# Kernel tuning notes

Hardware: AMD Instinct MI355X
Metric: run time of the kernel (lower is better)

## Reference

```python
import jax, jax.numpy as jnp
import numpy as np

N, E, IN_DIM, EMBED_DIM, HID_DIM = 10000, 320000, 128, 128, 64
NEG_SLOPE = 0.2


def setup_inputs() -> dict:
    key = jax.random.key(0)
    ks = jax.random.split(key, 7)
    x = jax.random.normal(ks[0], (N, IN_DIM), dtype=jnp.float32)
    edge_index = jax.random.randint(ks[1], (2, E), 0, N, dtype=jnp.int64)
    dense_w = jax.random.normal(ks[2], (IN_DIM, EMBED_DIM), dtype=jnp.float32) / np.sqrt(IN_DIM)
    dense_b = jnp.zeros((EMBED_DIM,), dtype=jnp.float32)
    gat_w = jax.random.normal(ks[3], (EMBED_DIM, HID_DIM), dtype=jnp.float32) / np.sqrt(EMBED_DIM)
    att_src = jax.random.normal(ks[4], (HID_DIM,), dtype=jnp.float32) * 0.1
    att_dst = jax.random.normal(ks[5], (HID_DIM,), dtype=jnp.float32) * 0.1
    gat_b = jnp.zeros((HID_DIM,), dtype=jnp.float32)
    return {"x": x, "edge_index": edge_index, "dense_w": dense_w, "dense_b": dense_b,
            "gat_w": gat_w, "att_src": att_src, "att_dst": att_dst, "gat_b": gat_b}


def reference(x, edge_index, dense_w, dense_b, gat_w, att_src, att_dst, gat_b):
    n = x.shape[0]
    # dense + relu
    h = jax.nn.relu(x @ dense_w + dense_b)            # [N, embed]
    # GATConv (heads=1): linear transform
    z = h @ gat_w                                     # [N, hid]
    # add self loops (PyG default)
    loops = jnp.arange(n, dtype=edge_index.dtype)
    src = jnp.concatenate([edge_index[0], loops])     # [E+N] message source j
    dst = jnp.concatenate([edge_index[1], loops])     # [E+N] message target i
    a_src = z @ att_src                               # [N]
    a_dst = z @ att_dst                               # [N]
    e = jax.nn.leaky_relu(a_src[src] + a_dst[dst], NEG_SLOPE)  # [E+N]
    # segment softmax over incoming edges of each target node
    m = jax.ops.segment_max(e, dst, num_segments=n)
    ex = jnp.exp(e - m[dst])
    denom = jax.ops.segment_sum(ex, dst, num_segments=n)
    alpha = ex / denom[dst]                           # [E+N]
    embed_x = jax.ops.segment_sum(alpha[:, None] * z[src], dst, num_segments=n) + gat_b  # [N, hid]
    # pairwise sigmoid similarity
    sim = jax.nn.sigmoid(embed_x @ embed_x.T)         # [N, N]
    return sim, embed_x
```

## Files before the change

### kernel.cpp

```cpp
#include <hip/hip_runtime.h>
#include <math.h>

#define N_NODES 10000
#define E_EDGES 320000
#define IN_DIM 128
#define EMB 128
#define HID 64
#define NEG_SLOPE 0.2f

typedef __attribute__((ext_vector_type(8))) short short8;
typedef __attribute__((ext_vector_type(4))) short short4_t;
typedef __attribute__((ext_vector_type(4))) float floatx4;
typedef __attribute__((ext_vector_type(4))) int   intx4;
typedef __attribute__((ext_vector_type(2))) int   intx2;

__device__ __forceinline__ short f2bf(float f) {
    unsigned u = __float_as_uint(f);
    unsigned r = u + 0x7fffu + ((u >> 16) & 1u);
    return (short)(r >> 16);
}

__device__ __forceinline__ float sigmoidf_fast(float v) {
    return __builtin_amdgcn_rcpf(1.f + __expf(-v));
}

__global__ __launch_bounds__(256) void dense_gat_kernel(
    const float* __restrict__ x, const float* __restrict__ dw,
    const float* __restrict__ db, const float* __restrict__ gw,
    const float* __restrict__ asv, const float* __restrict__ adv,
    float* __restrict__ z, float* __restrict__ a_src, float* __restrict__ a_dst)
{
    __shared__ float xs[16][IN_DIM];
    __shared__ float hs[16][EMB];
    __shared__ float wsm[32 * 128];
    const int t = threadIdx.x;
    const int row0 = blockIdx.x * 16;

    #pragma unroll
    for (int r = 0; r < 2; ++r) {
        const int idx = t + r * 256;
        const int row = idx >> 5, c4 = idx & 31;
        *(floatx4*)&xs[row][c4 * 4] =
            *(const floatx4*)&x[(row0 + row) * IN_DIM + c4 * 4];
    }

    const int col = t & 127, rb = (t >> 7) * 8;
    float acc[8];
    {
        const float bias = db[col];
        #pragma unroll
        for (int r = 0; r < 8; ++r) acc[r] = bias;
    }
    for (int ch = 0; ch < 4; ++ch) {
        __syncthreads();
        #pragma unroll
        for (int r = 0; r < 4; ++r) {
            const int idx = t + r * 256;
            const int row = idx >> 5, c4 = idx & 31;
            *(floatx4*)&wsm[row * 128 + c4 * 4] =
                *(const floatx4*)&dw[(ch * 32 + row) * EMB + c4 * 4];
        }
        __syncthreads();
        #pragma unroll
        for (int jg = 0; jg < 8; ++jg) {
            const int jb = jg * 4;
            floatx4 xr[8];
            #pragma unroll
            for (int r = 0; r < 8; ++r)
                xr[r] = *(const floatx4*)&xs[rb + r][ch * 32 + jb];
            float wv[4];
            #pragma unroll
            for (int k = 0; k < 4; ++k) wv[k] = wsm[(jb + k) * 128 + col];
            #pragma unroll
            for (int k = 0; k < 4; ++k)
                #pragma unroll
                for (int r = 0; r < 8; ++r) acc[r] = fmaf(xr[r][k], wv[k], acc[r]);
        }
    }
    #pragma unroll
    for (int r = 0; r < 8; ++r) hs[rb + r][col] = fmaxf(acc[r], 0.f);

    const int col2 = t & 63, rb2 = (t >> 6) * 4;
    float acc2[4] = {0.f, 0.f, 0.f, 0.f};
    for (int ch = 0; ch < 2; ++ch) {
        __syncthreads();
        #pragma unroll
        for (int r = 0; r < 4; ++r) {
            const int idx = t + r * 256;
            const int row = idx >> 4, c4 = idx & 15;
            *(floatx4*)&wsm[row * 64 + c4 * 4] =
                *(const floatx4*)&gw[(ch * 64 + row) * HID + c4 * 4];
        }
        __syncthreads();
        #pragma unroll
        for (int kg = 0; kg < 16; ++kg) {
            const int kb = kg * 4;
            floatx4 hr[4];
            #pragma unroll
            for (int r = 0; r < 4; ++r)
                hr[r] = *(const floatx4*)&hs[rb2 + r][ch * 64 + kb];
            float gv[4];
            #pragma unroll
            for (int k = 0; k < 4; ++k) gv[k] = wsm[(kb + k) * 64 + col2];
            #pragma unroll
            for (int k = 0; k < 4; ++k)
                #pragma unroll
                for (int r = 0; r < 4; ++r) acc2[r] = fmaf(hr[r][k], gv[k], acc2[r]);
        }
    }

    const float as_c = asv[col2], ad_c = adv[col2];
    #pragma unroll
    for (int r = 0; r < 4; ++r) {
        z[(row0 + rb2 + r) * HID + col2] = acc2[r];
        float ps = acc2[r] * as_c;
        float pd = acc2[r] * ad_c;
        #pragma unroll
        for (int off = 32; off > 0; off >>= 1) {
            ps += __shfl_down(ps, off, 64);
            pd += __shfl_down(pd, off, 64);
        }
        if ((t & 63) == 0) {
            a_src[row0 + rb2 + r] = ps;
            a_dst[row0 + rb2 + r] = pd;
        }
    }
}

__global__ __launch_bounds__(256) void count_kernel(
    const int* __restrict__ ei, int* __restrict__ cnt)
{
    const int e = blockIdx.x * blockDim.x + threadIdx.x;
    const int total = E_EDGES + N_NODES;
    if (e >= total) return;
    int s, d;
    if (e < E_EDGES) { s = ei[e]; d = ei[E_EDGES + e]; }
    else             { s = d = e - E_EDGES; }
    if ((unsigned)s >= N_NODES || (unsigned)d >= N_NODES) return;
    atomicAdd(&cnt[d], 1);
}

__global__ __launch_bounds__(256) void scan_kernel(
    const int* __restrict__ cnt, int* __restrict__ offs, int* __restrict__ cursor)
{
    __shared__ int scnt[10240];
    __shared__ int part[256];
    const int t = threadIdx.x;
    #pragma unroll
    for (int r = 0; r < 10; ++r) {
        const int i4 = t + r * 256;
        intx4 v = {0, 0, 0, 0};
        if (i4 < 2500) v = *(const intx4*)&cnt[i4 * 4];
        *(intx4*)&scnt[i4 * 4] = v;
    }
    __syncthreads();
    const int base = t * 40;
    int vals[40];
    int local = 0;
    #pragma unroll
    for (int i = 0; i < 40; ++i) { vals[i] = scnt[base + i]; local += vals[i]; }
    part[t] = local;
    __syncthreads();
    for (int off = 1; off < 256; off <<= 1) {
        const int v = (t >= off) ? part[t - off] : 0;
        __syncthreads();
        part[t] += v;
        __syncthreads();
    }
    int running = (t == 0) ? 0 : part[t - 1];
    #pragma unroll
    for (int i = 0; i < 40; ++i) {
        const int idx = base + i;
        if (idx < N_NODES) { offs[idx] = running; cursor[idx] = running; }
        running += vals[i];
    }
    if (t == 255) offs[N_NODES] = running;
}

__global__ __launch_bounds__(256) void scatter_kernel(
    const int* __restrict__ ei, const float* __restrict__ a_src,
    const float* __restrict__ a_dst, int* __restrict__ cursor,
    intx2* __restrict__ se)
{
    const int e = blockIdx.x * blockDim.x + threadIdx.x;
    const int total = E_EDGES + N_NODES;
    if (e >= total) return;
    int s, d;
    if (e < E_EDGES) { s = ei[e]; d = ei[E_EDGES + e]; }
    else             { s = d = e - E_EDGES; }
    if ((unsigned)s >= N_NODES || (unsigned)d >= N_NODES) return;
    float v = a_src[s] + a_dst[d];
    v = (v > 0.f) ? v : NEG_SLOPE * v;
    const float w = __expf(v);
    const int pos = atomicAdd(&cursor[d], 1);
    intx2 p;
    p[0] = s;
    p[1] = __float_as_int(w);
    se[pos] = p;
}

__global__ __launch_bounds__(256) void aggregate_kernel(
    const int* __restrict__ offs, const intx2* __restrict__ se,
    const float* __restrict__ z, const float* __restrict__ gb,
    float* __restrict__ emb)
{
    const int wid  = (blockIdx.x * blockDim.x + threadIdx.x) >> 6;
    const int lane = threadIdx.x & 63;
    if (wid >= N_NODES) return;
    const int g  = lane >> 4;
    const int c4 = (lane & 15) * 4;
    const int beg = offs[wid], end = offs[wid + 1];
    floatx4 acc = {0.f, 0.f, 0.f, 0.f};
    float sw = 0.f;
    for (int i = beg + g; i < end; i += 4) {
        const intx2 p = se[i];
        const floatx4 zv = *(const floatx4*)&z[p[0] * HID + c4];
        const float w = __int_as_float(p[1]);
        acc += zv * w;
        sw  += w;
    }
    #pragma unroll
    for (int off = 16; off <= 32; off <<= 1) {
        #pragma unroll
        for (int k = 0; k < 4; ++k) acc[k] += __shfl_xor(acc[k], off, 64);
        sw += __shfl_xor(sw, off, 64);
    }
    if (g == 0) {
        const floatx4 gv = *(const floatx4*)&gb[c4];
        floatx4 r;
        #pragma unroll
        for (int k = 0; k < 4; ++k) r[k] = acc[k] / sw + gv[k];
        *(floatx4*)&emb[wid * HID + c4] = r;
    }
}

#define SROW 72
#define SCR_STRIDE 133
__global__ __launch_bounds__(256) void sim_kernel(
    const float* __restrict__ emb, float* __restrict__ sim)
{
    __shared__ float smem[128 * SCR_STRIDE];
    short* const As = (short*)smem;
    short* const Bs = (short*)smem + 128 * SROW;
    const int t    = threadIdx.x;
    const int lane = t & 63;
    const int wave = t >> 6;
    const int wm   = (wave >> 1) * 64;
    const int wn   = (wave & 1) * 64;
    const int l15  = lane & 15;
    const int quad = lane >> 4;

    int bi, bj;
    {
        const int gx = blockIdx.x, gy = blockIdx.y;
        if (gy <= gx) { bi = gy; bj = gx; }
        else          { bi = 40 + gx; bj = 79 + gx - gy; }
    }

    #pragma unroll
    for (int round = 0; round < 8; ++round) {
        const int idx = t + round * 256;
        const int row = idx >> 4, c4 = idx & 15;
        int gr = bi * 128 + row; if (gr > N_NODES - 1) gr = N_NODES - 1;
        int gc = bj * 128 + row; if (gc > N_NODES - 1) gc = N_NODES - 1;
        const floatx4 a = *(const floatx4*)&emb[gr * HID + c4 * 4];
        const floatx4 b = *(const floatx4*)&emb[gc * HID + c4 * 4];
        short4_t sa, sb;
        #pragma unroll
        for (int j = 0; j < 4; ++j) { sa[j] = f2bf(a[j]); sb[j] = f2bf(b[j]); }
        *(short4_t*)&As[row * SROW + c4 * 4] = sa;
        *(short4_t*)&Bs[row * SROW + c4 * 4] = sb;
    }
    __syncthreads();

    short8 afrag[4][2];
    #pragma unroll
    for (int ti = 0; ti < 4; ++ti)
        #pragma unroll
        for (int ks = 0; ks < 2; ++ks)
            afrag[ti][ks] = *(const short8*)&As[(wm + ti * 16 + l15) * SROW +
                                                ks * 32 + quad * 8];

    floatx4 acc[4][4];
    const floatx4 zero = {0.f, 0.f, 0.f, 0.f};
    #pragma unroll
    for (int ti = 0; ti < 4; ++ti)
        #pragma unroll
        for (int tj = 0; tj < 4; ++tj) acc[ti][tj] = zero;

    #pragma unroll
    for (int tj = 0; tj < 4; ++tj) {
        const short8 bf0 = *(const short8*)&Bs[(wn + tj * 16 + l15) * SROW + quad * 8];
        const short8 bf1 = *(const short8*)&Bs[(wn + tj * 16 + l15) * SROW + 32 + quad * 8];
        #pragma unroll
        for (int ti = 0; ti < 4; ++ti) {
            acc[ti][tj] = __builtin_amdgcn_mfma_f32_16x16x32_bf16(
                afrag[ti][0], bf0, acc[ti][tj], 0, 0, 0);
            acc[ti][tj] = __builtin_amdgcn_mfma_f32_16x16x32_bf16(
                afrag[ti][1], bf1, acc[ti][tj], 0, 0, 0);
        }
    }
    __syncthreads();

    #pragma unroll
    for (int ti = 0; ti < 4; ++ti)
        #pragma unroll
        for (int reg = 0; reg < 4; ++reg)
            #pragma unroll
            for (int tj = 0; tj < 4; ++tj)
                smem[(wm + ti * 16 + quad * 4 + reg) * SCR_STRIDE +
                     wn + tj * 16 + l15] = sigmoidf_fast(acc[ti][tj][reg]);
    __syncthreads();

    #pragma unroll
    for (int round = 0; round < 16; ++round) {
        const int idx = t + round * 256;
        const int rr = idx >> 5, cq = idx & 31;
        const int grow = bi * 128 + rr;
        const int gcol = bj * 128 + cq * 4;
        if (grow < N_NODES && gcol < N_NODES) {
            const floatx4 v4 = *(const floatx4*)&smem[rr * SCR_STRIDE + cq * 4];
            *(floatx4*)&sim[(unsigned)grow * N_NODES + gcol] = v4;
        }
    }
    if (bi != bj) {
        #pragma unroll
        for (int round = 0; round < 16; ++round) {
            const int idx = t + round * 256;
            const int rr = idx >> 5, cq = idx & 31;
            const int trow = bj * 128 + rr;
            const int tcol = bi * 128 + cq * 4;
            if (trow < N_NODES && tcol < N_NODES) {
                floatx4 v4;
                #pragma unroll
                for (int m = 0; m < 4; ++m)
                    v4[m] = smem[(cq * 4 + m) * SCR_STRIDE + rr];
                *(floatx4*)&sim[(unsigned)trow * N_NODES + tcol] = v4;
            }
        }
    }
}

extern "C" void kernel_launch(void* const* d_in, const int* in_sizes, int n_in,
                              void* d_out, int out_size, void* d_ws, size_t ws_size,
                              hipStream_t stream)
{
    const float* x   = (const float*)d_in[0];
    const int*   ei  = (const int*)d_in[1];
    const float* dw  = (const float*)d_in[2];
    const float* db  = (const float*)d_in[3];
    const float* gw  = (const float*)d_in[4];
    const float* asv = (const float*)d_in[5];
    const float* adv = (const float*)d_in[6];
    const float* gb  = (const float*)d_in[7];

    float* out = (float*)d_out;
    float* sim = out;
    float* emb = out + (size_t)N_NODES * N_NODES;

    const size_t need = 1350002u * sizeof(float);
    float* ws = (ws_size >= need) ? (float*)d_ws : out;
    float* z      = ws;
    float* a_src  = ws + 640000;
    float* a_dst  = ws + 650000;
    int*   cnt    = (int*)(ws + 660000);
    int*   offs   = (int*)(ws + 670000);
    int*   cursor = (int*)(ws + 680001);
    intx2* se     = (intx2*)(ws + 690002);

    hipMemsetAsync(cnt, 0, N_NODES * sizeof(int), stream);

    dense_gat_kernel<<<N_NODES / 16, 256, 0, stream>>>(x, dw, db, gw, asv, adv,
                                                       z, a_src, a_dst);

    const int total_edges = E_EDGES + N_NODES;
    const int eb = (total_edges + 255) / 256;
    count_kernel<<<eb, 256, 0, stream>>>(ei, cnt);
    scan_kernel<<<1, 256, 0, stream>>>(cnt, offs, cursor);
    scatter_kernel<<<eb, 256, 0, stream>>>(ei, a_src, a_dst, cursor, se);
    aggregate_kernel<<<(N_NODES * 64 + 255) / 256, 256, 0, stream>>>(
        offs, se, z, gb, emb);

    dim3 grid(79, 40);
    sim_kernel<<<grid, 256, 0, stream>>>(emb, sim);
}
```

Before: 563.9 us.

## Fuse graph stages into one cooperative kernel and use nontemporal sim stores

Merges the dense/GAT projection, edge counting, scan, scatter and aggregation into a single cooperative kernel with grid-wide syncs. Dense work and edge counting run concurrently on disjoint blocks. This removes several launch gaps and lets the two independent stages overlap, with a fallback to the old multi-kernel path if the cooperative launch fails. The sim output writes also become nontemporal stores to reduce cache pollution from the large N×N result. Risks include the cost of grid sync, lower occupancy from the launch bounds, and the single-block scan idling the rest of the grid.

```diff
diff --git a/kernel.cpp b/kernel.cpp
--- a/kernel.cpp
+++ b/kernel.cpp
@@ -1,5 +1,8 @@
 #include <hip/hip_runtime.h>
+#include <hip/hip_cooperative_groups.h>
 #include <math.h>
+
+namespace cg = cooperative_groups;
 
 #define N_NODES 10000
 #define E_EDGES 320000
@@ -8,6 +11,9 @@
 #define HID 64
 #define NEG_SLOPE 0.2f
 
+#define COOP_BLOCKS 1024
+#define DG_BLOCKS 625
+
 typedef __attribute__((ext_vector_type(8))) short short8;
 typedef __attribute__((ext_vector_type(4))) short short4_t;
 typedef __attribute__((ext_vector_type(4))) float floatx4;
@@ -24,23 +30,23 @@
     return __builtin_amdgcn_rcpf(1.f + __expf(-v));
 }
 
-__global__ __launch_bounds__(256) void dense_gat_kernel(
+__device__ __forceinline__ void dense_gat_body(
+    float* __restrict__ smem,
+    int row0, int t,
     const float* __restrict__ x, const float* __restrict__ dw,
     const float* __restrict__ db, const float* __restrict__ gw,
     const float* __restrict__ asv, const float* __restrict__ adv,
     float* __restrict__ z, float* __restrict__ a_src, float* __restrict__ a_dst)
 {
-    __shared__ float xs[16][IN_DIM];
-    __shared__ float hs[16][EMB];
-    __shared__ float wsm[32 * 128];
-    const int t = threadIdx.x;
-    const int row0 = blockIdx.x * 16;
+    float* const xs  = smem;
+    float* const hs  = smem + 2048;
+    float* const wsm = smem + 4096;
 
     #pragma unroll
     for (int r = 0; r < 2; ++r) {
         const int idx = t + r * 256;
         const int row = idx >> 5, c4 = idx & 31;
-        *(floatx4*)&xs[row][c4 * 4] =
+        *(floatx4*)&xs[row * 128 + c4 * 4] =
             *(const floatx4*)&x[(row0 + row) * IN_DIM + c4 * 4];
     }
 
@@ -67,7 +73,7 @@
             floatx4 xr[8];
             #pragma unroll
             for (int r = 0; r < 8; ++r)
-                xr[r] = *(const floatx4*)&xs[rb + r][ch * 32 + jb];
+                xr[r] = *(const floatx4*)&xs[(rb + r) * 128 + ch * 32 + jb];
             float wv[4];
             #pragma unroll
             for (int k = 0; k < 4; ++k) wv[k] = wsm[(jb + k) * 128 + col];
@@ -78,7 +84,7 @@
         }
     }
     #pragma unroll
-    for (int r = 0; r < 8; ++r) hs[rb + r][col] = fmaxf(acc[r], 0.f);
+    for (int r = 0; r < 8; ++r) hs[(rb + r) * 128 + col] = fmaxf(acc[r], 0.f);
 
     const int col2 = t & 63, rb2 = (t >> 6) * 4;
     float acc2[4] = {0.f, 0.f, 0.f, 0.f};
@@ -98,7 +104,7 @@
             floatx4 hr[4];
             #pragma unroll
             for (int r = 0; r < 4; ++r)
-                hr[r] = *(const floatx4*)&hs[rb2 + r][ch * 64 + kb];
+                hr[r] = *(const floatx4*)&hs[(rb2 + r) * 128 + ch * 64 + kb];
             float gv[4];
             #pragma unroll
             for (int k = 0; k < 4; ++k) gv[k] = wsm[(kb + k) * 64 + col2];
@@ -127,38 +133,33 @@
     }
 }
 
-__global__ __launch_bounds__(256) void count_kernel(
-    const int* __restrict__ ei, int* __restrict__ cnt)
-{
-    const int e = blockIdx.x * blockDim.x + threadIdx.x;
+__device__ __forceinline__ void count_body(
+    int tid, int nth, const int* __restrict__ ei, int* __restrict__ cnt)
+{
     const int total = E_EDGES + N_NODES;
-    if (e >= total) return;
-    int s, d;
-    if (e < E_EDGES) { s = ei[e]; d = ei[E_EDGES + e]; }
-    else             { s = d = e - E_EDGES; }
-    if ((unsigned)s >= N_NODES || (unsigned)d >= N_NODES) return;
-    atomicAdd(&cnt[d], 1);
-}
-
-__global__ __launch_bounds__(256) void scan_kernel(
+    for (int e = tid; e < total; e += nth) {
+        int s, d;
+        if (e < E_EDGES) { s = ei[e]; d = ei[E_EDGES + e]; }
+        else             { s = d = e - E_EDGES; }
+        if ((unsigned)s >= N_NODES || (unsigned)d >= N_NODES) continue;
+        atomicAdd(&cnt[d], 1);
+    }
+}
+
+__device__ __forceinline__ void scan_body(
+    int* __restrict__ part, int t,
     const int* __restrict__ cnt, int* __restrict__ offs, int* __restrict__ cursor)
 {
-    __shared__ int scnt[10240];
-    __shared__ int part[256];
-    const int t = threadIdx.x;
-    #pragma unroll
-    for (int r = 0; r < 10; ++r) {
-        const int i4 = t + r * 256;
-        intx4 v = {0, 0, 0, 0};
-        if (i4 < 2500) v = *(const intx4*)&cnt[i4 * 4];
-        *(intx4*)&scnt[i4 * 4] = v;
-    }
-    __syncthreads();
     const int base = t * 40;
     int vals[40];
     int local = 0;
     #pragma unroll
-    for (int i = 0; i < 40; ++i) { vals[i] = scnt[base + i]; local += vals[i]; }
+    for (int i = 0; i < 40; ++i) {
+        const int idx = base + i;
+        const int c = (idx < N_NODES) ? cnt[idx] : 0;
+        vals[i] = c;
+        local += c;
+    }
     part[t] = local;
     __syncthreads();
     for (int off = 1; off < 256; off <<= 1) {
@@ -177,36 +178,33 @@
     if (t == 255) offs[N_NODES] = running;
 }
 
-__global__ __launch_bounds__(256) void scatter_kernel(
-    const int* __restrict__ ei, const float* __restrict__ a_src,
-    const float* __restrict__ a_dst, int* __restrict__ cursor,
-    intx2* __restrict__ se)
-{
-    const int e = blockIdx.x * blockDim.x + threadIdx.x;
+__device__ __forceinline__ void scatter_body(
+    int tid, int nth, const int* __restrict__ ei,
+    const float* __restrict__ a_src, const float* __restrict__ a_dst,
+    int* __restrict__ cursor, intx2* __restrict__ se)
+{
     const int total = E_EDGES + N_NODES;
-    if (e >= total) return;
-    int s, d;
-    if (e < E_EDGES) { s = ei[e]; d = ei[E_EDGES + e]; }
-    else             { s = d = e - E_EDGES; }
-    if ((unsigned)s >= N_NODES || (unsigned)d >= N_NODES) return;
-    float v = a_src[s] + a_dst[d];
-    v = (v > 0.f) ? v : NEG_SLOPE * v;
-    const float w = __expf(v);
-    const int pos = atomicAdd(&cursor[d], 1);
-    intx2 p;
-    p[0] = s;
-    p[1] = __float_as_int(w);
-    se[pos] = p;
-}
-
-__global__ __launch_bounds__(256) void aggregate_kernel(
-    const int* __restrict__ offs, const intx2* __restrict__ se,
+    for (int e = tid; e < total; e += nth) {
+        int s, d;
+        if (e < E_EDGES) { s = ei[e]; d = ei[E_EDGES + e]; }
+        else             { s = d = e - E_EDGES; }
+        if ((unsigned)s >= N_NODES || (unsigned)d >= N_NODES) continue;
+        float v = a_src[s] + a_dst[d];
+        v = (v > 0.f) ? v : NEG_SLOPE * v;
+        const float w = __expf(v);
+        const int pos = atomicAdd(&cursor[d], 1);
+        intx2 p;
+        p[0] = s;
+        p[1] = __float_as_int(w);
+        se[pos] = p;
+    }
+}
+
+__device__ __forceinline__ void aggregate_body(
+    int wid, int lane, const int* __restrict__ offs, const intx2* __restrict__ se,
     const float* __restrict__ z, const float* __restrict__ gb,
     float* __restrict__ emb)
 {
-    const int wid  = (blockIdx.x * blockDim.x + threadIdx.x) >> 6;
-    const int lane = threadIdx.x & 63;
-    if (wid >= N_NODES) return;
     const int g  = lane >> 4;
     const int c4 = (lane & 15) * 4;
     const int beg = offs[wid], end = offs[wid + 1];
@@ -234,6 +232,87 @@
     }
 }
 
+__global__ __launch_bounds__(256, 4) void fused_graph_kernel(
+    const float* __restrict__ x, const float* __restrict__ dw,
+    const float* __restrict__ db, const float* __restrict__ gw,
+    const float* __restrict__ asv, const float* __restrict__ adv,
+    const int* __restrict__ ei, const float* __restrict__ gb,
+    float* __restrict__ z, float* __restrict__ a_src, float* __restrict__ a_dst,
+    int* __restrict__ cnt, int* __restrict__ offs, int* __restrict__ cursor,
+    intx2* __restrict__ se, float* __restrict__ emb)
+{
+    __shared__ float smem[8192];
+    cg::grid_group grid = cg::this_grid();
+    const int b = blockIdx.x;
+    const int t = threadIdx.x;
+
+    if (b < DG_BLOCKS) {
+        dense_gat_body(smem, b * 16, t, x, dw, db, gw, asv, adv, z, a_src, a_dst);
+    } else {
+        const int tid = (b - DG_BLOCKS) * 256 + t;
+        count_body(tid, (COOP_BLOCKS - DG_BLOCKS) * 256, ei, cnt);
+    }
+    grid.sync();
+
+    if (b == 0) scan_body((int*)smem, t, cnt, offs, cursor);
+    grid.sync();
+
+    scatter_body(b * 256 + t, COOP_BLOCKS * 256, ei, a_src, a_dst, cursor, se);
+    grid.sync();
+
+    {
+        const int lane = t & 63;
+        const int wave_glob = (b * 256 + t) >> 6;
+        for (int wid = wave_glob; wid < N_NODES; wid += COOP_BLOCKS * 4)
+            aggregate_body(wid, lane, offs, se, z, gb, emb);
+    }
+}
+
+__global__ __launch_bounds__(256) void dense_gat_kernel(
+    const float* __restrict__ x, const float* __restrict__ dw,
+    const float* __restrict__ db, const float* __restrict__ gw,
+    const float* __restrict__ asv, const float* __restrict__ adv,
+    float* __restrict__ z, float* __restrict__ a_src, float* __restrict__ a_dst)
+{
+    __shared__ float smem[8192];
+    dense_gat_body(smem, blockIdx.x * 16, threadIdx.x,
+                   x, dw, db, gw, asv, adv, z, a_src, a_dst);
+}
+
+__global__ __launch_bounds__(256) void count_kernel(
+    const int* __restrict__ ei, int* __restrict__ cnt)
+{
+    count_body(blockIdx.x * blockDim.x + threadIdx.x,
+               gridDim.x * blockDim.x, ei, cnt);
+}
+
+__global__ __launch_bounds__(256) void scan_kernel(
+    const int* __restrict__ cnt, int* __restrict__ offs, int* __restrict__ cursor)
+{
+    __shared__ int part[256];
+    scan_body(part, threadIdx.x, cnt, offs, cursor);
+}
+
+__global__ __launch_bounds__(256) void scatter_kernel(
+    const int* __restrict__ ei, const float* __restrict__ a_src,
+    const float* __restrict__ a_dst, int* __restrict__ cursor,
+    intx2* __restrict__ se)
+{
+    scatter_body(blockIdx.x * blockDim.x + threadIdx.x,
+                 gridDim.x * blockDim.x, ei, a_src, a_dst, cursor, se);
+}
+
+__global__ __launch_bounds__(256) void aggregate_kernel(
+    const int* __restrict__ offs, const intx2* __restrict__ se,
+    const float* __restrict__ z, const float* __restrict__ gb,
+    float* __restrict__ emb)
+{
+    const int wid  = (blockIdx.x * blockDim.x + threadIdx.x) >> 6;
+    const int lane = threadIdx.x & 63;
+    if (wid >= N_NODES) return;
+    aggregate_body(wid, lane, offs, se, z, gb, emb);
+}
+
 #define SROW 72
 #define SCR_STRIDE 133
 __global__ __launch_bounds__(256) void sim_kernel(
@@ -320,7 +399,8 @@
         const int gcol = bj * 128 + cq * 4;
         if (grow < N_NODES && gcol < N_NODES) {
             const floatx4 v4 = *(const floatx4*)&smem[rr * SCR_STRIDE + cq * 4];
-            *(floatx4*)&sim[(unsigned)grow * N_NODES + gcol] = v4;
+            __builtin_nontemporal_store(
+                v4, (floatx4*)&sim[(unsigned)grow * N_NODES + gcol]);
         }
     }
     if (bi != bj) {
@@ -335,7 +415,8 @@
                 #pragma unroll
                 for (int m = 0; m < 4; ++m)
                     v4[m] = smem[(cq * 4 + m) * SCR_STRIDE + rr];
-                *(floatx4*)&sim[(unsigned)trow * N_NODES + tcol] = v4;
+                __builtin_nontemporal_store(
+                    v4, (floatx4*)&sim[(unsigned)trow * N_NODES + tcol]);
             }
         }
     }
@@ -370,16 +451,30 @@
 
     hipMemsetAsync(cnt, 0, N_NODES * sizeof(int), stream);
 
-    dense_gat_kernel<<<N_NODES / 16, 256, 0, stream>>>(x, dw, db, gw, asv, adv,
-                                                       z, a_src, a_dst);
-
-    const int total_edges = E_EDGES + N_NODES;
-    const int eb = (total_edges + 255) / 256;
-    count_kernel<<<eb, 256, 0, stream>>>(ei, cnt);
-    scan_kernel<<<1, 256, 0, stream>>>(cnt, offs, cursor);
-    scatter_kernel<<<eb, 256, 0, stream>>>(ei, a_src, a_dst, cursor, se);
-    aggregate_kernel<<<(N_NODES * 64 + 255) / 256, 256, 0, stream>>>(
-        offs, se, z, gb, emb);
+    {
+        const float* xa = x; const float* dwa = dw; const float* dba = db;
+        const float* gwa = gw; const float* asa = asv; const float* ada = adv;
+        const int* eia = ei; const float* gba = gb;
+        float* za = z; float* asra = a_src; float* adsa = a_dst;
+        int* cnta = cnt; int* offsa = offs; int* cura = cursor;
+        intx2* sea = se; float* emba = emb;
+        void* args[] = {&xa, &dwa, &dba, &gwa, &asa, &ada, &eia, &gba,
+                        &za, &asra, &adsa, &cnta, &offsa, &cura, &sea, &emba};
+        hipError_t err = hipLaunchCooperativeKernel(
+            (const void*)fused_graph_kernel, dim3(COOP_BLOCKS), dim3(256),
+            args, 0, stream);
+        if (err != hipSuccess) {
+            const int total_edges = E_EDGES + N_NODES;
+            const int eb = (total_edges + 255) / 256;
+            dense_gat_kernel<<<DG_BLOCKS, 256, 0, stream>>>(
+                x, dw, db, gw, asv, adv, z, a_src, a_dst);
+            count_kernel<<<eb, 256, 0, stream>>>(ei, cnt);
+            scan_kernel<<<1, 256, 0, stream>>>(cnt, offs, cursor);
+            scatter_kernel<<<eb, 256, 0, stream>>>(ei, a_src, a_dst, cursor, se);
+            aggregate_kernel<<<(N_NODES * 64 + 255) / 256, 256, 0, stream>>>(
+                offs, se, z, gb, emb);
+        }
+    }
 
     dim3 grid(79, 40);
     sim_kernel<<<grid, 256, 0, stream>>>(emb, sim);
```

Result: slower. 939.9 us (+66.7%).
